# Optimization experiments

Hardware: AMD Instinct MI355X
Metric: run time of the kernel (lower is better)

## Reference

```python
import jax, jax.numpy as jnp
import numpy as np

N0, IN, HID, OUT, H = 262144, 128, 256, 256, 4
S1, S2, S3 = 32768, 4096, 512
E1, E2, E3 = 327680, 40960, 5120
NEG_SLOPE, BN_EPS = 0.2, 1e-5


def setup_inputs() -> dict:
    key = jax.random.key(0)
    ks = iter(jax.random.split(key, 64))
    def nrm(shape, fan_in):
        return jax.random.normal(next(ks), shape, jnp.float32) / np.sqrt(fan_in).astype(np.float32)
    inp = {"x": jax.random.normal(next(ks), (N0, IN), jnp.float32)}
    # (in_dim, full_out_dim, concat) per layer; per-head channels c = full/H if concat else full
    dims = [(IN, H * HID, True), (H * HID, H * HID, True), (H * HID, OUT, False)]
    for i, (din, dfull, concat) in enumerate(dims, 1):
        c = dfull // H if concat else dfull
        hc = H * c
        inp[f"w_src{i}"] = nrm((hc, din), din)
        inp[f"w_dst{i}"] = nrm((hc, din), din)
        inp[f"att_src{i}"] = nrm((H, c), c)
        inp[f"att_dst{i}"] = nrm((H, c), c)
        inp[f"b_conv{i}"] = jnp.zeros((dfull,), jnp.float32)
        inp[f"w_skip{i}"] = nrm((dfull, din), din)
        inp[f"b_skip{i}"] = jnp.zeros((dfull,), jnp.float32)
        inp[f"gamma{i}"] = jnp.ones((dfull,), jnp.float32)
        inp[f"beta{i}"] = jnp.zeros((dfull,), jnp.float32)
    for i, (E, nsrc, ndst) in enumerate([(E1, N0, S1), (E2, S1, S2), (E3, S2, S3)], 1):
        inp[f"edge_src{i}"] = jax.random.randint(next(ks), (E,), 0, nsrc, dtype=jnp.int32)
        inp[f"edge_dst{i}"] = jax.random.randint(next(ks), (E,), 0, ndst, dtype=jnp.int32)
    inp["size1"], inp["size2"], inp["size3"] = S1, S2, S3
    return inp


def gat_layer(x_all, size, src, dst, w_src, w_dst, a_src, a_dst, b, concat):
    c = w_src.shape[0] // H
    h_src = (x_all @ w_src.T).reshape(-1, H, c)        # [N_src,H,C]
    h_dst = (x_all[:size] @ w_dst.T).reshape(-1, H, c)  # [N_dst,H,C]
    al_src = jnp.einsum('nhc,hc->nh', h_src, a_src)
    al_dst = jnp.einsum('nhc,hc->nh', h_dst, a_dst)
    loop = jnp.arange(size, dtype=src.dtype)  # PyG add_self_loops on dst nodes
    s = jnp.concatenate([src, loop])
    d = jnp.concatenate([dst, loop])
    logits = jax.nn.leaky_relu(al_src[s] + al_dst[d], NEG_SLOPE)  # [E,H]
    m = jax.ops.segment_max(logits, d, num_segments=size)
    e = jnp.exp(logits - m[d])
    denom = jax.ops.segment_sum(e, d, num_segments=size)
    alpha = e / (denom[d] + 1e-16)
    out = jax.ops.segment_sum(h_src[s] * alpha[:, :, None], d, num_segments=size)
    out = out.reshape(size, H * c) if concat else out.mean(axis=1)
    return out + b


def batchnorm(x, g, b):
    mu = x.mean(0)
    var = x.var(0)
    return (x - mu) * jax.lax.rsqrt(var + BN_EPS) * g + b


def reference(x,
              w_src1, w_dst1, att_src1, att_dst1, b_conv1, w_skip1, b_skip1, gamma1, beta1,
              w_src2, w_dst2, att_src2, att_dst2, b_conv2, w_skip2, b_skip2, gamma2, beta2,
              w_src3, w_dst3, att_src3, att_dst3, b_conv3, w_skip3, b_skip3, gamma3, beta3,
              edge_src1, edge_dst1, edge_src2, edge_dst2, edge_src3, edge_dst3,
              size1, size2, size3):
    layers = [
        (size1, edge_src1, edge_dst1, w_src1, w_dst1, att_src1, att_dst1, b_conv1, w_skip1, b_skip1, gamma1, beta1, True),
        (size2, edge_src2, edge_dst2, w_src2, w_dst2, att_src2, att_dst2, b_conv2, w_skip2, b_skip2, gamma2, beta2, True),
        (size3, edge_src3, edge_dst3, w_src3, w_dst3, att_src3, att_dst3, b_conv3, w_skip3, b_skip3, gamma3, beta3, False),
    ]
    for (size, src, dst, ws, wd, a_s, a_d, bc, wsk, bsk, g, be, concat) in layers:
        x_t = x[:size]
        h = gat_layer(x, size, src, dst, ws, wd, a_s, a_d, bc, concat)
        h = h + x_t @ wsk.T + bsk
        h = batchnorm(h, g, be)
        x = jax.nn.elu(h)
    return x
```

## Files before the change

kernel.cpp:

```cpp
#include <hip/hip_runtime.h>
#include <math.h>

constexpr int N0 = 262144, S1 = 32768, S2 = 4096, S3 = 512;
constexpr int E1 = 327680, E2 = 40960, E3 = 5120;
constexpr float NEG = 0.2f, BN_EPS = 1e-5f;

typedef __attribute__((ext_vector_type(8))) short short8;
typedef __attribute__((ext_vector_type(4))) float f32x4;

__device__ __forceinline__ float lrelu(float x) { return x > 0.f ? x : NEG * x; }

__device__ __forceinline__ unsigned short f2b(float f) {
    unsigned int u = __float_as_uint(f);
    return (unsigned short)((u + 0x7FFFu + ((u >> 16) & 1u)) >> 16);
}
__device__ __forceinline__ float b2f(unsigned short u) {
    return __uint_as_float(((unsigned int)u) << 16);
}
__device__ __forceinline__ void ld4(const float* __restrict__ p, float* o) {
    float4 v = *(const float4*)p;
    o[0] = v.x; o[1] = v.y; o[2] = v.z; o[3] = v.w;
}

__device__ __forceinline__ void gload_lds16(const unsigned short* g, unsigned short* l) {
    __builtin_amdgcn_global_load_lds(
        (const __attribute__((address_space(1))) unsigned int*)g,
        (__attribute__((address_space(3))) unsigned int*)l, 16, 0, 0);
}

struct PrepArgs {
    const float* att[6]; const float* wf[6]; float* v[6];
    const float* csrc[6]; unsigned short* cdst[6];
    int* zptr; int zn4;
};

__global__ void prep_kernel(PrepArgs a)
{
    int b = blockIdx.x, t = threadIdx.x;
    if (b < 68) {
        int f, cb;
        if (b < 2)       { f = 0; cb = b; }
        else if (b < 4)  { f = 1; cb = b - 2; }
        else if (b < 20) { f = 2; cb = b - 4; }
        else if (b < 36) { f = 3; cb = b - 20; }
        else if (b < 52) { f = 4; cb = b - 36; }
        else             { f = 5; cb = b - 52; }
        int din = (f < 2) ? 128 : 1024;
        int idx = cb * 256 + t;
        int h = idx / din, k = idx - h * din;
        const float* ar = a.att[f] + h * 256;
        const float* wr = a.wf[f] + (size_t)(h * 256) * din + k;
        float acc = 0.f;
        for (int j = 0; j < 256; ++j) acc += ar[j] * wr[(size_t)j * din];
        a.v[f][idx] = acc;
    } else if (b < 124) {
        int c = b - 68, j, ob;
        if (c < 2)       { j = 0; ob = c; }
        else if (c < 4)  { j = 1; ob = c - 2; }
        else if (c < 20) { j = 2; ob = c - 4; }
        else if (c < 36) { j = 3; ob = c - 20; }
        else if (c < 40) { j = 4; ob = c - 36; }
        else             { j = 5; ob = c - 40; }
        long base = (long)ob * 65536;
        if (j < 5) {
            const float* src = a.csrc[j];
            unsigned short* dst = a.cdst[j];
            for (int it = 0; it < 64; ++it) {
                long e = base + (long)(it * 256 + t) * 4;
                float4 v = *(const float4*)(src + e);
                ushort4 u;
                u.x = f2b(v.x); u.y = f2b(v.y); u.z = f2b(v.z); u.w = f2b(v.w);
                *(ushort4*)(dst + e) = u;
            }
        } else {
            const float* src = a.csrc[5];
            unsigned short* dst = a.cdst[5];
            for (int it = 0; it < 64; ++it) {
                long e = base + (long)(it * 256 + t) * 4;
                int row = (int)(e >> 12);
                int hk = (int)(e & 4095);
                int h = hk >> 10, k = hk & 1023;
                float4 v = *(const float4*)(src + ((size_t)(h * 256 + row) << 10) + k);
                ushort4 u;
                u.x = f2b(0.25f * v.x); u.y = f2b(0.25f * v.y);
                u.z = f2b(0.25f * v.z); u.w = f2b(0.25f * v.w);
                *(ushort4*)(dst + e) = u;
            }
        }
    } else {
        int i = (b - 124) * 256 + t;
        if (i < a.zn4) ((int4*)a.zptr)[i] = make_int4(0, 0, 0, 0);
    }
}

struct CsrArgs {
    const int* edst[3];
    int* counts[3]; int* offsets[3]; int* cursor[3]; int* elist[3];
    int sizes[3];
};

__global__ void count_all(CsrArgs a)
{
    int id = blockIdx.x * 256 + threadIdx.x;
    int L, e;
    if (id < E1)           { L = 0; e = id; }
    else if (id < E1 + E2) { L = 1; e = id - E1; }
    else if (id < E1 + E2 + E3) { L = 2; e = id - E1 - E2; }
    else return;
    atomicAdd(&a.counts[L][a.edst[L][e]], 1);
}

__global__ void scan_all(CsrArgs a)
{
    __shared__ int lds[1024];
    int L = blockIdx.x;
    int size = a.sizes[L];
    const int* counts = a.counts[L];
    int* offsets = a.offsets[L];
    int* cursor = a.cursor[L];
    int t = threadIdx.x;
    int chunk = (size + 1023) >> 10;
    int begin = t * chunk;
    int end = begin + chunk; if (end > size) end = size;
    if (begin > size) begin = size;
    int s = 0;
    if ((chunk & 3) == 0) {
        for (int i = begin; i < end; i += 4) {
            int4 v = *(const int4*)(counts + i);
            s += v.x + v.y + v.z + v.w;
        }
    } else {
        for (int i = begin; i < end; ++i) s += counts[i];
    }
    lds[t] = s;
    __syncthreads();
    for (int d = 1; d < 1024; d <<= 1) {
        int v = (t >= d) ? lds[t - d] : 0;
        __syncthreads();
        lds[t] += v;
        __syncthreads();
    }
    int base = (t > 0) ? lds[t - 1] : 0;
    for (int i = begin; i < end; ++i) {
        offsets[i] = base; cursor[i] = base;
        base += counts[i];
    }
    if (t == 1023) offsets[size] = lds[1023];
}

__global__ void scatter_all(CsrArgs a)
{
    int id = blockIdx.x * 256 + threadIdx.x;
    int L, e;
    if (id < E1)           { L = 0; e = id; }
    else if (id < E1 + E2) { L = 1; e = id - E1; }
    else if (id < E1 + E2 + E3) { L = 2; e = id - E1 - E2; }
    else return;
    int p = atomicAdd(&a.cursor[L][a.edst[L][e]], 1);
    a.elist[L][p] = e;
}

__global__ void al128f_kernel(const float* __restrict__ x, const float* __restrict__ vs,
                              const float* __restrict__ vd, unsigned short* __restrict__ xb,
                              float* __restrict__ als, float* __restrict__ ald, int n, int ndst)
{
    int lane = threadIdx.x & 63;
    int wave = (blockIdx.x * 256 + threadIdx.x) >> 6;
    int nw = (gridDim.x * 256) >> 6;
    int j32 = lane & 31, half = lane >> 5;
    float vsr[4][4], vdr[4][4];
    #pragma unroll
    for (int h = 0; h < 4; ++h) {
        ld4(vs + h * 128 + j32 * 4, vsr[h]);
        ld4(vd + h * 128 + j32 * 4, vdr[h]);
    }
    for (long node = (long)wave * 2 + half; node < n; node += (long)nw * 2) {
        float4 xv = *(const float4*)(x + node * 128 + j32 * 4);
        ushort4 u;
        u.x = f2b(xv.x); u.y = f2b(xv.y); u.z = f2b(xv.z); u.w = f2b(xv.w);
        *(ushort4*)(xb + node * 128 + j32 * 4) = u;
        float xf[4] = { xv.x, xv.y, xv.z, xv.w };
        float a[4], bv[4];
        bool isd = node < ndst;
        #pragma unroll
        for (int h = 0; h < 4; ++h)
            a[h] = xf[0]*vsr[h][0] + xf[1]*vsr[h][1] + xf[2]*vsr[h][2] + xf[3]*vsr[h][3];
        if (isd) {
            #pragma unroll
            for (int h = 0; h < 4; ++h)
                bv[h] = xf[0]*vdr[h][0] + xf[1]*vdr[h][1] + xf[2]*vdr[h][2] + xf[3]*vdr[h][3];
        }
        #pragma unroll
        for (int off = 16; off > 0; off >>= 1) {
            #pragma unroll
            for (int h = 0; h < 4; ++h) a[h] += __shfl_xor(a[h], off);
            if (isd)
                #pragma unroll
                for (int h = 0; h < 4; ++h) bv[h] += __shfl_xor(bv[h], off);
        }
        if (j32 == 0) {
            *(float4*)(als + node * 4) = make_float4(a[0], a[1], a[2], a[3]);
            if (isd) *(float4*)(ald + node * 4) = make_float4(bv[0], bv[1], bv[2], bv[3]);
        }
    }
}

__global__ void al1024d_kernel(const unsigned short* __restrict__ xb,
                               const float* __restrict__ vs, const float* __restrict__ vd,
                               float* __restrict__ als, float* __restrict__ ald,
                               int nsrc, int ndst, int bsrc)
{
    bool isdst = (int)blockIdx.x >= bsrc;
    const float* v = isdst ? vd : vs;
    float* al = isdst ? ald : als;
    int n = isdst ? ndst : nsrc;
    int b0 = isdst ? blockIdx.x - bsrc : blockIdx.x;
    int nb = isdst ? gridDim.x - bsrc : bsrc;
    int lane = threadIdx.x & 63;
    int wave = (b0 * 256 + threadIdx.x) >> 6;
    int nwaves = (nb * 256) >> 6;
    float vr[4][16];
    #pragma unroll
    for (int h = 0; h < 4; ++h)
        #pragma unroll
        for (int it = 0; it < 2; ++it) {
            ld4(v + h * 1024 + it * 512 + lane * 8,     &vr[h][it * 8]);
            ld4(v + h * 1024 + it * 512 + lane * 8 + 4, &vr[h][it * 8 + 4]);
        }
    for (long node = wave; node < n; node += nwaves) {
        const unsigned short* xr = xb + node * 1024;
        float a[4] = {0.f, 0.f, 0.f, 0.f};
        #pragma unroll
        for (int it = 0; it < 2; ++it) {
            short8 u = *(const short8*)(xr + it * 512 + lane * 8);
            #pragma unroll
            for (int j = 0; j < 8; ++j) {
                float xv = b2f((unsigned short)u[j]);
                #pragma unroll
                for (int h = 0; h < 4; ++h) a[h] += xv * vr[h][it * 8 + j];
            }
        }
        #pragma unroll
        for (int off = 32; off > 0; off >>= 1)
            #pragma unroll
            for (int h = 0; h < 4; ++h) a[h] += __shfl_xor(a[h], off);
        if (lane == 0) *(float4*)(al + node * 4) = make_float4(a[0], a[1], a[2], a[3]);
    }
}

__global__ void mdnw_kernel(const float* __restrict__ als, const float* __restrict__ ald,
                            const int* __restrict__ offsets, const int* __restrict__ elist,
                            const int* __restrict__ esrc, int size,
                            float* __restrict__ aself, float* __restrict__ walpha)
{
    int d = blockIdx.x * 4 + (threadIdx.x >> 6);
    if (d >= size) return;
    int lane = threadIdx.x & 63;
    float ad[4], sl[4], q[4];
    ld4(ald + 4 * (size_t)d, ad);
    ld4(als + 4 * (size_t)d, q);
    #pragma unroll
    for (int h = 0; h < 4; ++h) sl[h] = lrelu(q[h] + ad[h]);
    int beg = offsets[d], deg = offsets[d + 1] - beg;
    float m[4] = { sl[0], sl[1], sl[2], sl[3] };
    for (int p = lane; p < deg; p += 64) {
        int s = esrc[elist[beg + p]];
        ld4(als + 4 * (size_t)s, q);
        #pragma unroll
        for (int h = 0; h < 4; ++h) m[h] = fmaxf(m[h], lrelu(q[h] + ad[h]));
    }
    #pragma unroll
    for (int off = 32; off > 0; off >>= 1)
        #pragma unroll
        for (int h = 0; h < 4; ++h) m[h] = fmaxf(m[h], __shfl_xor(m[h], off));
    float dn[4] = {0.f, 0.f, 0.f, 0.f};
    for (int p = lane; p < deg; p += 64) {
        int s = esrc[elist[beg + p]];
        ld4(als + 4 * (size_t)s, q);
        #pragma unroll
        for (int h = 0; h < 4; ++h) dn[h] += expf(lrelu(q[h] + ad[h]) - m[h]);
    }
    #pragma unroll
    for (int off = 32; off > 0; off >>= 1)
        #pragma unroll
        for (int h = 0; h < 4; ++h) dn[h] += __shfl_xor(dn[h], off);
    float r[4];
    #pragma unroll
    for (int h = 0; h < 4; ++h)
        r[h] = 1.f / (dn[h] + expf(sl[h] - m[h]) + 1e-16f);
    if (lane == 0) {
        float4 w;
        w.x = expf(sl[0] - m[0]) * r[0];
        w.y = expf(sl[1] - m[1]) * r[1];
        w.z = expf(sl[2] - m[2]) * r[2];
        w.w = expf(sl[3] - m[3]) * r[3];
        *(float4*)(aself + 4 * (size_t)d) = w;
    }
    for (int p = lane; p < deg; p += 64) {
        int e = elist[beg + p];
        int s = esrc[e];
        ld4(als + 4 * (size_t)s, q);
        float4 w;
        w.x = expf(lrelu(q[0] + ad[0]) - m[0]) * r[0];
        w.y = expf(lrelu(q[1] + ad[1]) - m[1]) * r[1];
        w.z = expf(lrelu(q[2] + ad[2]) - m[2]) * r[2];
        w.w = expf(lrelu(q[3] + ad[3]) - m[3]) * r[3];
        *(float4*)(walpha + 4 * (size_t)e) = w;
    }
}

__global__ void agg128_kernel(const unsigned short* __restrict__ xb, const float* __restrict__ walpha,
                              const float* __restrict__ aself,
                              const int* __restrict__ offsets, const int* __restrict__ elist,
                              const int* __restrict__ esrc, unsigned short* __restrict__ aggb)
{
    int d = blockIdx.x, lane = threadIdx.x;
    int beg = offsets[d], end = offsets[d + 1];
    float w[4], acc[4][2];
    ld4(aself + 4 * (size_t)d, w);
    {
        unsigned int u = *(const unsigned int*)(xb + (size_t)d * 128 + lane * 2);
        float x0 = b2f((unsigned short)(u & 0xFFFF)), x1 = b2f((unsigned short)(u >> 16));
        #pragma unroll
        for (int h = 0; h < 4; ++h) { acc[h][0] = w[h] * x0; acc[h][1] = w[h] * x1; }
    }
    for (int p = beg; p < end; ++p) {
        int e = elist[p];
        int s = esrc[e];
        ld4(walpha + 4 * (size_t)e, w);
        unsigned int u = *(const unsigned int*)(xb + (size_t)s * 128 + lane * 2);
        float x0 = b2f((unsigned short)(u & 0xFFFF)), x1 = b2f((unsigned short)(u >> 16));
        #pragma unroll
        for (int h = 0; h < 4; ++h) { acc[h][0] += w[h] * x0; acc[h][1] += w[h] * x1; }
    }
    unsigned int* og = (unsigned int*)(aggb + (size_t)d * 512);
    #pragma unroll
    for (int h = 0; h < 4; ++h)
        og[h * 64 + lane] = (unsigned int)f2b(acc[h][0]) | ((unsigned int)f2b(acc[h][1]) << 16);
}

__global__ void agg1024_kernel(const unsigned short* __restrict__ xb, const float* __restrict__ walpha,
                               const float* __restrict__ aself,
                               const int* __restrict__ offsets, const int* __restrict__ elist,
                               const int* __restrict__ esrc, unsigned short* __restrict__ aggb)
{
    int d = blockIdx.x, t = threadIdx.x;
    int beg = offsets[d], end = offsets[d + 1];
    float w[4], acc[4][4];
    ld4(aself + 4 * (size_t)d, w);
    {
        ushort4 u = *(const ushort4*)(xb + (size_t)d * 1024 + t * 4);
        float xv[4] = { b2f(u.x), b2f(u.y), b2f(u.z), b2f(u.w) };
        #pragma unroll
        for (int h = 0; h < 4; ++h)
            #pragma unroll
            for (int j = 0; j < 4; ++j) acc[h][j] = w[h] * xv[j];
    }
    for (int p = beg; p < end; ++p) {
        int e = elist[p];
        int s = esrc[e];
        ld4(walpha + 4 * (size_t)e, w);
        ushort4 u = *(const ushort4*)(xb + (size_t)s * 1024 + t * 4);
        float xv[4] = { b2f(u.x), b2f(u.y), b2f(u.z), b2f(u.w) };
        #pragma unroll
        for (int h = 0; h < 4; ++h)
            #pragma unroll
            for (int j = 0; j < 4; ++j) acc[h][j] += w[h] * xv[j];
    }
    unsigned short* og = aggb + (size_t)d * 4096;
    #pragma unroll
    for (int h = 0; h < 4; ++h) {
        ushort4 u;
        u.x = f2b(acc[h][0]); u.y = f2b(acc[h][1]);
        u.z = f2b(acc[h][2]); u.w = f2b(acc[h][3]);
        *(ushort4*)(og + h * 1024 + t * 4) = u;
    }
}

#define SWZ(r, c) ((((c) ^ (((r) >> 1) & 3)) << 3))

template<int BM, int BN>
__global__ __launch_bounds__(256) void gemm2_kernel(
    const unsigned short* __restrict__ A1, int lda1, const unsigned short* __restrict__ W1, int K1,
    const unsigned short* __restrict__ A2, int lda2, const unsigned short* __restrict__ W2, int K2,
    int hs2, int cph2,
    unsigned short* __restrict__ C, int N,
    float* __restrict__ bnsum, float* __restrict__ bnsq)
{
    constexpr int WM = BM / 2, WN = BN / 2;
    constexpr int TM = WM / 16, TN = WN / 16;
    constexpr int APASS = (BM * 4) / 256, BPASS = (BN * 4) / 256;
    __shared__ __align__(16) unsigned short As[BM * 32];
    __shared__ __align__(16) unsigned short Bs[BN * 32];
    __shared__ float sbn[2 * BN];
    int tid = threadIdx.x;
    int n0 = blockIdx.x * BN, m0 = blockIdx.y * BM;
    int l = tid & 63, l16 = l & 15, kq = l >> 4;
    int wid = tid >> 6, wr = wid >> 1, wc = wid & 1;

    f32x4 acc[TM][TN];
    #pragma unroll
    for (int mi = 0; mi < TM; ++mi)
        #pragma unroll
        for (int ni = 0; ni < TN; ++ni) acc[mi][ni] = (f32x4){0.f, 0.f, 0.f, 0.f};

    #pragma unroll
    for (int ph = 0; ph < 2; ++ph) {
        const unsigned short* Ap = ph ? A2 + (size_t)m0 * lda2 + (cph2 ? (size_t)(n0 / cph2) * hs2 : 0)
                                      : A1 + (size_t)m0 * lda1;
        int lda = ph ? lda2 : lda1;
        const unsigned short* Wp = ph ? W2 + (size_t)n0 * K2 : W1 + (size_t)n0 * K1;
        int ldw = ph ? K2 : K1;
        int K = ph ? K2 : K1;
        for (int k0 = 0; k0 < K; k0 += 32) {
            #pragma unroll
            for (int ps = 0; ps < APASS; ++ps) {
                int sbase = ps * 256 + wid * 64;
                int s = sbase + l;
                int r = s >> 2, cc = s & 3;
                gload_lds16(Ap + (size_t)r * lda + k0 + ((cc ^ ((r >> 1) & 3)) << 3),
                            &As[(size_t)sbase * 8]);
            }
            #pragma unroll
            for (int ps = 0; ps < BPASS; ++ps) {
                int sbase = ps * 256 + wid * 64;
                int s = sbase + l;
                int r = s >> 2, cc = s & 3;
                gload_lds16(Wp + (size_t)r * ldw + k0 + ((cc ^ ((r >> 1) & 3)) << 3),
                            &Bs[(size_t)sbase * 8]);
            }
            __syncthreads();
            short8 af[TM], bfr[TN];
            #pragma unroll
            for (int mi = 0; mi < TM; ++mi) {
                int r = wr * WM + mi * 16 + l16;
                af[mi] = *(const short8*)&As[r * 32 + SWZ(r, kq)];
            }
            #pragma unroll
            for (int ni = 0; ni < TN; ++ni) {
                int r = wc * WN + ni * 16 + l16;
                bfr[ni] = *(const short8*)&Bs[r * 32 + SWZ(r, kq)];
            }
            #pragma unroll
            for (int mi = 0; mi < TM; ++mi)
                #pragma unroll
                for (int ni = 0; ni < TN; ++ni)
                    acc[mi][ni] = __builtin_amdgcn_mfma_f32_16x16x32_bf16(
                        af[mi], bfr[ni], acc[mi][ni], 0, 0, 0);
            __syncthreads();
        }
    }

    if (tid < 2 * BN) sbn[tid] = 0.f;
    __syncthreads();

    #pragma unroll
    for (int ni = 0; ni < TN; ++ni) {
        int col = wc * WN + ni * 16 + l16;
        float s = 0.f, q = 0.f;
        #pragma unroll
        for (int mi = 0; mi < TM; ++mi) {
            int rowb = wr * WM + mi * 16 + (kq << 2);
            #pragma unroll
            for (int r = 0; r < 4; ++r) {
                float v = acc[mi][ni][r];
                C[(size_t)(m0 + rowb + r) * N + n0 + col] = f2b(v);
                s += v; q += v * v;
            }
        }
        atomicAdd(&sbn[col * 2 + 0], s);
        atomicAdd(&sbn[col * 2 + 1], q);
    }
    __syncthreads();
    if (tid < BN) {
        atomicAdd(&bnsum[n0 + tid], sbn[tid * 2 + 0]);
        atomicAdd(&bnsq[n0 + tid], sbn[tid * 2 + 1]);
    }
}

__global__ __launch_bounds__(256) void gemm3_splitk(
    const unsigned short* __restrict__ A1, const unsigned short* __restrict__ W1,
    const unsigned short* __restrict__ A2, const unsigned short* __restrict__ W2,
    float* __restrict__ Cpart)
{
    constexpr int BM = 64, BN = 64, WM = 32, WN = 32, TM = 2, TN = 2;
    __shared__ __align__(16) unsigned short As[BM * 32];
    __shared__ __align__(16) unsigned short Bs[BN * 32];
    int tid = threadIdx.x;
    int n0 = blockIdx.x * BN, m0 = blockIdx.y * BM;
    int z = blockIdx.z;
    int ph = (z >= 2);
    int ks = ph ? (z - 2) * 512 : z * 512;
    const unsigned short* Ap = ph ? A2 + (size_t)m0 * 4096 : A1 + (size_t)m0 * 1024;
    const unsigned short* Wp = ph ? W2 + (size_t)n0 * 4096 : W1 + (size_t)n0 * 1024;
    int lda = ph ? 4096 : 1024;
    int l = tid & 63, l16 = l & 15, kq = l >> 4;
    int wid = tid >> 6, wr = wid >> 1, wc = wid & 1;

    f32x4 acc[TM][TN];
    #pragma unroll
    for (int mi = 0; mi < TM; ++mi)
        #pragma unroll
        for (int ni = 0; ni < TN; ++ni) acc[mi][ni] = (f32x4){0.f, 0.f, 0.f, 0.f};

    for (int k0 = ks; k0 < ks + 512; k0 += 32) {
        {
            int sbase = wid * 64;
            int s = sbase + l;
            int r = s >> 2, cc = s & 3;
            gload_lds16(Ap + (size_t)r * lda + k0 + ((cc ^ ((r >> 1) & 3)) << 3),
                        &As[(size_t)sbase * 8]);
            gload_lds16(Wp + (size_t)r * lda + k0 + ((cc ^ ((r >> 1) & 3)) << 3),
                        &Bs[(size_t)sbase * 8]);
        }
        __syncthreads();
        short8 af[TM], bfr[TN];
        #pragma unroll
        for (int mi = 0; mi < TM; ++mi) {
            int r = wr * WM + mi * 16 + l16;
            af[mi] = *(const short8*)&As[r * 32 + SWZ(r, kq)];
        }
        #pragma unroll
        for (int ni = 0; ni < TN; ++ni) {
            int r = wc * WN + ni * 16 + l16;
            bfr[ni] = *(const short8*)&Bs[r * 32 + SWZ(r, kq)];
        }
        #pragma unroll
        for (int mi = 0; mi < TM; ++mi)
            #pragma unroll
            for (int ni = 0; ni < TN; ++ni)
                acc[mi][ni] = __builtin_amdgcn_mfma_f32_16x16x32_bf16(
                    af[mi], bfr[ni], acc[mi][ni], 0, 0, 0);
        __syncthreads();
    }

    float* Cz = Cpart + (size_t)z * S3 * 256;
    #pragma unroll
    for (int ni = 0; ni < TN; ++ni) {
        int col = wc * WN + ni * 16 + l16;
        #pragma unroll
        for (int mi = 0; mi < TM; ++mi) {
            int rowb = wr * WM + mi * 16 + (kq << 2);
            #pragma unroll
            for (int r = 0; r < 4; ++r)
                Cz[(size_t)(m0 + rowb + r) * 256 + n0 + col] = acc[mi][ni][r];
        }
    }
}

__global__ void bnstat3_kernel(const float* __restrict__ Cpart, float* __restrict__ hb32,
                               float* __restrict__ bnsum, float* __restrict__ bnsq)
{
    int c = threadIdx.x;
    int r0 = blockIdx.x * 64;
    float s = 0.f, q = 0.f;
    for (int r = r0; r < r0 + 64; ++r) {
        float v = 0.f;
        #pragma unroll
        for (int z = 0; z < 10; ++z)
            v += Cpart[((size_t)z * S3 + r) * 256 + c];
        hb32[(size_t)r * 256 + c] = v;
        s += v; q += v * v;
    }
    atomicAdd(&bnsum[c], s);
    atomicAdd(&bnsq[c], q);
}

__global__ void norm_elu_bb(const unsigned short* __restrict__ h,
                            const float* __restrict__ sum, const float* __restrict__ sq,
                            const float* __restrict__ gamma, const float* __restrict__ beta,
                            unsigned short* __restrict__ out, int N, float invM, long total)
{
    long i = ((long)blockIdx.x * 256 + threadIdx.x) * 4;
    if (i >= total) return;
    int c = (int)(i % N);
    float4 sm = *(const float4*)(sum + c);
    float4 qq = *(const float4*)(sq + c);
    float4 gm = *(const float4*)(gamma + c);
    float4 bt = *(const float4*)(beta + c);
    float mu0 = sm.x * invM, mu1 = sm.y * invM, mu2 = sm.z * invM, mu3 = sm.w * invM;
    float sc0 = gm.x * rsqrtf(qq.x * invM - mu0 * mu0 + BN_EPS);
    float sc1 = gm.y * rsqrtf(qq.y * invM - mu1 * mu1 + BN_EPS);
    float sc2 = gm.z * rsqrtf(qq.z * invM - mu2 * mu2 + BN_EPS);
    float sc3 = gm.w * rsqrtf(qq.w * invM - mu3 * mu3 + BN_EPS);
    float sh0 = bt.x - mu0 * sc0, sh1 = bt.y - mu1 * sc1;
    float sh2 = bt.z - mu2 * sc2, sh3 = bt.w - mu3 * sc3;
    ushort4 u = *(const ushort4*)(h + i);
    float v0 = b2f(u.x) * sc0 + sh0;
    float v1 = b2f(u.y) * sc1 + sh1;
    float v2 = b2f(u.z) * sc2 + sh2;
    float v3 = b2f(u.w) * sc3 + sh3;
    v0 = v0 > 0.f ? v0 : expm1f(v0);
    v1 = v1 > 0.f ? v1 : expm1f(v1);
    v2 = v2 > 0.f ? v2 : expm1f(v2);
    v3 = v3 > 0.f ? v3 : expm1f(v3);
    ushort4 o;
    o.x = f2b(v0); o.y = f2b(v1); o.z = f2b(v2); o.w = f2b(v3);
    *(ushort4*)(out + i) = o;
}

__global__ void norm_elu_ff(const float* __restrict__ h,
                            const float* __restrict__ sum, const float* __restrict__ sq,
                            const float* __restrict__ gamma, const float* __restrict__ beta,
                            float* __restrict__ out, int N, float invM, long total)
{
    long i = ((long)blockIdx.x * 256 + threadIdx.x) * 4;
    if (i >= total) return;
    int c = (int)(i % N);
    float4 sm = *(const float4*)(sum + c);
    float4 qq = *(const float4*)(sq + c);
    float4 gm = *(const float4*)(gamma + c);
    float4 bt = *(const float4*)(beta + c);
    float mu0 = sm.x * invM, mu1 = sm.y * invM, mu2 = sm.z * invM, mu3 = sm.w * invM;
    float sc0 = gm.x * rsqrtf(qq.x * invM - mu0 * mu0 + BN_EPS);
    float sc1 = gm.y * rsqrtf(qq.y * invM - mu1 * mu1 + BN_EPS);
    float sc2 = gm.z * rsqrtf(qq.z * invM - mu2 * mu2 + BN_EPS);
    float sc3 = gm.w * rsqrtf(qq.w * invM - mu3 * mu3 + BN_EPS);
    float4 hv = *(const float4*)(h + i);
    float4 o;
    o.x = hv.x * sc0 + (bt.x - mu0 * sc0);
    o.y = hv.y * sc1 + (bt.y - mu1 * sc1);
    o.z = hv.z * sc2 + (bt.z - mu2 * sc2);
    o.w = hv.w * sc3 + (bt.w - mu3 * sc3);
    o.x = o.x > 0.f ? o.x : expm1f(o.x);
    o.y = o.y > 0.f ? o.y : expm1f(o.y);
    o.z = o.z > 0.f ? o.z : expm1f(o.z);
    o.w = o.w > 0.f ? o.w : expm1f(o.w);
    *(float4*)(out + i) = o;
}

extern "C" void kernel_launch(void* const* d_in, const int* in_sizes, int n_in,
                              void* d_out, int out_size, void* d_ws, size_t ws_size,
                              hipStream_t stream)
{
    const float* x = (const float*)d_in[0];
    auto P = [&](int layer, int slot) -> const float* {
        return (const float*)d_in[1 + (layer - 1) * 9 + slot];
    };
    const int* edge_src[3] = { (const int*)d_in[28], (const int*)d_in[30], (const int*)d_in[32] };
    const int* edge_dst[3] = { (const int*)d_in[29], (const int*)d_in[31], (const int*)d_in[33] };

    char* wsb = (char*)d_ws;
    size_t off = 0;
    auto alloc = [&](size_t bytes) -> void* {
        void* p = wsb + off;
        off = (off + bytes + 255) & ~(size_t)255;
        return p;
    };
    unsigned short* xb0   = (unsigned short*)alloc((size_t)N0 * 128 * 2);
    unsigned short* x1b   = (unsigned short*)alloc((size_t)S1 * 1024 * 2);
    unsigned short* x2b   = (unsigned short*)alloc((size_t)S2 * 1024 * 2);
    unsigned short* hb    = (unsigned short*)alloc((size_t)S1 * 1024 * 2);
    unsigned short* aggb  = (unsigned short*)alloc((size_t)S2 * 4096 * 2);
    unsigned short* wskipb[3] = {
        (unsigned short*)alloc(131072 * 2),
        (unsigned short*)alloc(1048576 * 2),
        (unsigned short*)alloc(262144 * 2) };
    unsigned short* wsrcb[3] = {
        (unsigned short*)alloc(131072 * 2),
        (unsigned short*)alloc(1048576 * 2),
        (unsigned short*)alloc(1048576 * 2) };
    float* vbuf[6];
    vbuf[0] = (float*)alloc(512 * 4);
    vbuf[1] = (float*)alloc(512 * 4);
    vbuf[2] = (float*)alloc(4096 * 4);
    vbuf[3] = (float*)alloc(4096 * 4);
    vbuf[4] = (float*)alloc(4096 * 4);
    vbuf[5] = (float*)alloc(4096 * 4);
    float* als     = (float*)alloc((size_t)N0 * 4 * 4);
    float* ald     = (float*)alloc((size_t)S1 * 4 * 4);
    float* aself   = (float*)alloc((size_t)S1 * 4 * 4);
    float* walpha  = (float*)alloc((size_t)E1 * 4 * 4);
    float* Cpart   = (float*)alloc((size_t)10 * S3 * 256 * 4);
    float* hb32    = (float*)alloc((size_t)S3 * 256 * 4);
    int* offsets3[3] = { (int*)alloc((S1 + 1) * 4), (int*)alloc((S2 + 1) * 4), (int*)alloc((S3 + 1) * 4) };
    int* cursor3 [3] = { (int*)alloc(S1 * 4), (int*)alloc(S2 * 4), (int*)alloc(S3 * 4) };
    int* elist3  [3] = { (int*)alloc(E1 * 4), (int*)alloc(E2 * 4), (int*)alloc(E3 * 4) };
    int zn = S1 + S2 + S3 + 6 * 1024;
    int* zreg = (int*)alloc((size_t)zn * 4);
    int* counts[3] = { zreg, zreg + S1, zreg + S1 + S2 };
    float* bnsum[3] = { (float*)(zreg + S1 + S2 + S3),
                        (float*)(zreg + S1 + S2 + S3 + 2048),
                        (float*)(zreg + S1 + S2 + S3 + 4096) };
    float* bnsq[3]  = { bnsum[0] + 1024, bnsum[1] + 1024, bnsum[2] + 1024 };

    PrepArgs pa;
    for (int L = 0; L < 3; ++L) {
        pa.att[2 * L]     = P(L + 1, 2); pa.wf[2 * L]     = P(L + 1, 0); pa.v[2 * L]     = vbuf[2 * L];
        pa.att[2 * L + 1] = P(L + 1, 3); pa.wf[2 * L + 1] = P(L + 1, 1); pa.v[2 * L + 1] = vbuf[2 * L + 1];
    }
    pa.csrc[0] = P(1, 5); pa.cdst[0] = wskipb[0];
    pa.csrc[1] = P(1, 0); pa.cdst[1] = wsrcb[0];
    pa.csrc[2] = P(2, 5); pa.cdst[2] = wskipb[1];
    pa.csrc[3] = P(2, 0); pa.cdst[3] = wsrcb[1];
    pa.csrc[4] = P(3, 5); pa.cdst[4] = wskipb[2];
    pa.csrc[5] = P(3, 0); pa.cdst[5] = wsrcb[2];
    pa.zptr = zreg; pa.zn4 = zn / 4;
    prep_kernel<<<167, 256, 0, stream>>>(pa);

    CsrArgs ca;
    for (int L = 0; L < 3; ++L) {
        ca.edst[L] = edge_dst[L];
        ca.counts[L] = counts[L]; ca.offsets[L] = offsets3[L];
        ca.cursor[L] = cursor3[L]; ca.elist[L] = elist3[L];
    }
    ca.sizes[0] = S1; ca.sizes[1] = S2; ca.sizes[2] = S3;
    count_all<<<(E1 + E2 + E3) / 256, 256, 0, stream>>>(ca);
    scan_all<<<3, 1024, 0, stream>>>(ca);
    scatter_all<<<(E1 + E2 + E3) / 256, 256, 0, stream>>>(ca);

    al128f_kernel<<<2048, 256, 0, stream>>>(x, vbuf[0], vbuf[1], xb0, als, ald, N0, S1);
    mdnw_kernel<<<(S1 + 3) / 4, 256, 0, stream>>>(als, ald, offsets3[0], elist3[0], edge_src[0],
                                                  S1, aself, walpha);
    agg128_kernel<<<S1, 64, 0, stream>>>(xb0, walpha, aself, offsets3[0], elist3[0], edge_src[0], aggb);
    gemm2_kernel<128, 128><<<dim3(1024 / 128, S1 / 128), 256, 0, stream>>>(
        xb0, 128, wskipb[0], 128,
        aggb, 512, wsrcb[0], 128, 128, 256,
        hb, 1024, bnsum[0], bnsq[0]);
    norm_elu_bb<<<(int)(((long)S1 * 1024 / 4 + 255) / 256), 256, 0, stream>>>(
        hb, bnsum[0], bnsq[0], P(1, 7), P(1, 8), x1b, 1024, 1.f / S1, (long)S1 * 1024);

    al1024d_kernel<<<576, 256, 0, stream>>>(x1b, vbuf[2], vbuf[3], als, ald, S1, S2, 512);
    mdnw_kernel<<<(S2 + 3) / 4, 256, 0, stream>>>(als, ald, offsets3[1], elist3[1], edge_src[1],
                                                  S2, aself, walpha);
    agg1024_kernel<<<S2, 256, 0, stream>>>(x1b, walpha, aself, offsets3[1], elist3[1], edge_src[1], aggb);
    gemm2_kernel<64, 64><<<dim3(1024 / 64, S2 / 64), 256, 0, stream>>>(
        x1b, 1024, wskipb[1], 1024,
        aggb, 4096, wsrcb[1], 1024, 1024, 256,
        hb, 1024, bnsum[1], bnsq[1]);
    norm_elu_bb<<<(int)(((long)S2 * 1024 / 4 + 255) / 256), 256, 0, stream>>>(
        hb, bnsum[1], bnsq[1], P(2, 7), P(2, 8), x2b, 1024, 1.f / S2, (long)S2 * 1024);

    al1024d_kernel<<<72, 256, 0, stream>>>(x2b, vbuf[4], vbuf[5], als, ald, S2, S3, 64);
    mdnw_kernel<<<(S3 + 3) / 4, 256, 0, stream>>>(als, ald, offsets3[2], elist3[2], edge_src[2],
                                                  S3, aself, walpha);
    agg1024_kernel<<<S3, 256, 0, stream>>>(x2b, walpha, aself, offsets3[2], elist3[2], edge_src[2], aggb);
    gemm3_splitk<<<dim3(256 / 64, S3 / 64, 10), 256, 0, stream>>>(
        x2b, wskipb[2], aggb, wsrcb[2], Cpart);
    bnstat3_kernel<<<8, 256, 0, stream>>>(Cpart, hb32, bnsum[2], bnsq[2]);
    norm_elu_ff<<<(int)(((long)S3 * 256 / 4 + 255) / 256), 256, 0, stream>>>(
        hb32, bnsum[2], bnsq[2], P(3, 7), P(3, 8), (float*)d_out, 256, 1.f / S3, (long)S3 * 256);
}
```

Baseline: 539.6 us.

## Store source ids in CSR, swizzle GEMM tile order, widen norm-ELU per thread

The CSR scatter now writes each edge's source node id directly in place of the edge id. This removes the double indirection esrc[elist[p]] in the softmax and aggregation kernels. Attention weights are stored in CSR order, so aggregation reads them contiguously instead of by scattered edge index. Separately, the GEMM block index is swizzled in groups of 8, likely to spread neighbouring tiles across XCDs for cache locality, and norm_elu_bb handles 8 elements per thread with half the grid.

```diff
diff --git a/kernel.cpp b/kernel.cpp
--- a/kernel.cpp
+++ b/kernel.cpp
@@ -94,8 +94,8 @@
 }
 
 struct CsrArgs {
-    const int* edst[3];
-    int* counts[3]; int* offsets[3]; int* cursor[3]; int* elist[3];
+    const int* edst[3]; const int* esrc[3];
+    int* counts[3]; int* offsets[3]; int* cursor[3]; int* slist[3];
     int sizes[3];
 };
 
@@ -157,7 +157,7 @@
     else if (id < E1 + E2 + E3) { L = 2; e = id - E1 - E2; }
     else return;
     int p = atomicAdd(&a.cursor[L][a.edst[L][e]], 1);
-    a.elist[L][p] = e;
+    a.slist[L][p] = a.esrc[L][e];
 }
 
 __global__ void al128f_kernel(const float* __restrict__ x, const float* __restrict__ vs,
@@ -249,9 +249,8 @@
 }
 
 __global__ void mdnw_kernel(const float* __restrict__ als, const float* __restrict__ ald,
-                            const int* __restrict__ offsets, const int* __restrict__ elist,
-                            const int* __restrict__ esrc, int size,
-                            float* __restrict__ aself, float* __restrict__ walpha)
+                            const int* __restrict__ offsets, const int* __restrict__ slist,
+                            int size, float* __restrict__ aself, float* __restrict__ walpha)
 {
     int d = blockIdx.x * 4 + (threadIdx.x >> 6);
     if (d >= size) return;
@@ -264,7 +263,7 @@
     int beg = offsets[d], deg = offsets[d + 1] - beg;
     float m[4] = { sl[0], sl[1], sl[2], sl[3] };
     for (int p = lane; p < deg; p += 64) {
-        int s = esrc[elist[beg + p]];
+        int s = slist[beg + p];
         ld4(als + 4 * (size_t)s, q);
         #pragma unroll
         for (int h = 0; h < 4; ++h) m[h] = fmaxf(m[h], lrelu(q[h] + ad[h]));
@@ -275,7 +274,7 @@
         for (int h = 0; h < 4; ++h) m[h] = fmaxf(m[h], __shfl_xor(m[h], off));
     float dn[4] = {0.f, 0.f, 0.f, 0.f};
     for (int p = lane; p < deg; p += 64) {
-        int s = esrc[elist[beg + p]];
+        int s = slist[beg + p];
         ld4(als + 4 * (size_t)s, q);
         #pragma unroll
         for (int h = 0; h < 4; ++h) dn[h] += expf(lrelu(q[h] + ad[h]) - m[h]);
@@ -297,22 +296,21 @@
         *(float4*)(aself + 4 * (size_t)d) = w;
     }
     for (int p = lane; p < deg; p += 64) {
-        int e = elist[beg + p];
-        int s = esrc[e];
+        int s = slist[beg + p];
         ld4(als + 4 * (size_t)s, q);
         float4 w;
         w.x = expf(lrelu(q[0] + ad[0]) - m[0]) * r[0];
         w.y = expf(lrelu(q[1] + ad[1]) - m[1]) * r[1];
         w.z = expf(lrelu(q[2] + ad[2]) - m[2]) * r[2];
         w.w = expf(lrelu(q[3] + ad[3]) - m[3]) * r[3];
-        *(float4*)(walpha + 4 * (size_t)e) = w;
+        *(float4*)(walpha + 4 * (size_t)(beg + p)) = w;
     }
 }
 
 __global__ void agg128_kernel(const unsigned short* __restrict__ xb, const float* __restrict__ walpha,
                               const float* __restrict__ aself,
-                              const int* __restrict__ offsets, const int* __restrict__ elist,
-                              const int* __restrict__ esrc, unsigned short* __restrict__ aggb)
+                              const int* __restrict__ offsets, const int* __restrict__ slist,
+                              unsigned short* __restrict__ aggb)
 {
     int d = blockIdx.x, lane = threadIdx.x;
     int beg = offsets[d], end = offsets[d + 1];
@@ -325,9 +323,8 @@
         for (int h = 0; h < 4; ++h) { acc[h][0] = w[h] * x0; acc[h][1] = w[h] * x1; }
     }
     for (int p = beg; p < end; ++p) {
-        int e = elist[p];
-        int s = esrc[e];
-        ld4(walpha + 4 * (size_t)e, w);
+        int s = slist[p];
+        ld4(walpha + 4 * (size_t)p, w);
         unsigned int u = *(const unsigned int*)(xb + (size_t)s * 128 + lane * 2);
         float x0 = b2f((unsigned short)(u & 0xFFFF)), x1 = b2f((unsigned short)(u >> 16));
         #pragma unroll
@@ -341,8 +338,8 @@
 
 __global__ void agg1024_kernel(const unsigned short* __restrict__ xb, const float* __restrict__ walpha,
                                const float* __restrict__ aself,
-                               const int* __restrict__ offsets, const int* __restrict__ elist,
-                               const int* __restrict__ esrc, unsigned short* __restrict__ aggb)
+                               const int* __restrict__ offsets, const int* __restrict__ slist,
+                               unsigned short* __restrict__ aggb)
 {
     int d = blockIdx.x, t = threadIdx.x;
     int beg = offsets[d], end = offsets[d + 1];
@@ -357,9 +354,8 @@
             for (int j = 0; j < 4; ++j) acc[h][j] = w[h] * xv[j];
     }
     for (int p = beg; p < end; ++p) {
-        int e = elist[p];
-        int s = esrc[e];
-        ld4(walpha + 4 * (size_t)e, w);
+        int s = slist[p];
+        ld4(walpha + 4 * (size_t)p, w);
         ushort4 u = *(const ushort4*)(xb + (size_t)s * 1024 + t * 4);
         float xv[4] = { b2f(u.x), b2f(u.y), b2f(u.z), b2f(u.w) };
         #pragma unroll
@@ -394,7 +390,12 @@
     __shared__ __align__(16) unsigned short Bs[BN * 32];
     __shared__ float sbn[2 * BN];
     int tid = threadIdx.x;
-    int n0 = blockIdx.x * BN, m0 = blockIdx.y * BM;
+    int gx = gridDim.x;
+    int nwg = gx * gridDim.y;
+    int bid = blockIdx.y * gx + blockIdx.x;
+    int cpx = nwg >> 3;
+    int swz = (bid & 7) * cpx + (bid >> 3);
+    int n0 = (swz % gx) * BN, m0 = (swz / gx) * BM;
     int l = tid & 63, l16 = l & 15, kq = l >> 4;
     int wid = tid >> 6, wr = wid >> 1, wc = wid & 1;
 
@@ -571,32 +572,36 @@
                             const float* __restrict__ gamma, const float* __restrict__ beta,
                             unsigned short* __restrict__ out, int N, float invM, long total)
 {
-    long i = ((long)blockIdx.x * 256 + threadIdx.x) * 4;
-    if (i >= total) return;
-    int c = (int)(i % N);
-    float4 sm = *(const float4*)(sum + c);
-    float4 qq = *(const float4*)(sq + c);
-    float4 gm = *(const float4*)(gamma + c);
-    float4 bt = *(const float4*)(beta + c);
-    float mu0 = sm.x * invM, mu1 = sm.y * invM, mu2 = sm.z * invM, mu3 = sm.w * invM;
-    float sc0 = gm.x * rsqrtf(qq.x * invM - mu0 * mu0 + BN_EPS);
-    float sc1 = gm.y * rsqrtf(qq.y * invM - mu1 * mu1 + BN_EPS);
-    float sc2 = gm.z * rsqrtf(qq.z * invM - mu2 * mu2 + BN_EPS);
-    float sc3 = gm.w * rsqrtf(qq.w * invM - mu3 * mu3 + BN_EPS);
-    float sh0 = bt.x - mu0 * sc0, sh1 = bt.y - mu1 * sc1;
-    float sh2 = bt.z - mu2 * sc2, sh3 = bt.w - mu3 * sc3;
-    ushort4 u = *(const ushort4*)(h + i);
-    float v0 = b2f(u.x) * sc0 + sh0;
-    float v1 = b2f(u.y) * sc1 + sh1;
-    float v2 = b2f(u.z) * sc2 + sh2;
-    float v3 = b2f(u.w) * sc3 + sh3;
-    v0 = v0 > 0.f ? v0 : expm1f(v0);
-    v1 = v1 > 0.f ? v1 : expm1f(v1);
-    v2 = v2 > 0.f ? v2 : expm1f(v2);
-    v3 = v3 > 0.f ? v3 : expm1f(v3);
-    ushort4 o;
-    o.x = f2b(v0); o.y = f2b(v1); o.z = f2b(v2); o.w = f2b(v3);
-    *(ushort4*)(out + i) = o;
+    long i0 = ((long)blockIdx.x * 256 + threadIdx.x) * 8;
+    if (i0 >= total) return;
+    #pragma unroll
+    for (int g = 0; g < 2; ++g) {
+        long i = i0 + g * 4;
+        int c = (int)(i % N);
+        float4 sm = *(const float4*)(sum + c);
+        float4 qq = *(const float4*)(sq + c);
+        float4 gm = *(const float4*)(gamma + c);
+        float4 bt = *(const float4*)(beta + c);
+        float mu0 = sm.x * invM, mu1 = sm.y * invM, mu2 = sm.z * invM, mu3 = sm.w * invM;
+        float sc0 = gm.x * rsqrtf(qq.x * invM - mu0 * mu0 + BN_EPS);
+        float sc1 = gm.y * rsqrtf(qq.y * invM - mu1 * mu1 + BN_EPS);
+        float sc2 = gm.z * rsqrtf(qq.z * invM - mu2 * mu2 + BN_EPS);
+        float sc3 = gm.w * rsqrtf(qq.w * invM - mu3 * mu3 + BN_EPS);
+        float sh0 = bt.x - mu0 * sc0, sh1 = bt.y - mu1 * sc1;
+        float sh2 = bt.z - mu2 * sc2, sh3 = bt.w - mu3 * sc3;
+        ushort4 u = *(const ushort4*)(h + i);
+        float v0 = b2f(u.x) * sc0 + sh0;
+        float v1 = b2f(u.y) * sc1 + sh1;
+        float v2 = b2f(u.z) * sc2 + sh2;
+        float v3 = b2f(u.w) * sc3 + sh3;
+        v0 = v0 > 0.f ? v0 : expm1f(v0);
+        v1 = v1 > 0.f ? v1 : expm1f(v1);
+        v2 = v2 > 0.f ? v2 : expm1f(v2);
+        v3 = v3 > 0.f ? v3 : expm1f(v3);
+        ushort4 o;
+        o.x = f2b(v0); o.y = f2b(v1); o.z = f2b(v2); o.w = f2b(v3);
+        *(ushort4*)(out + i) = o;
+    }
 }
 
 __global__ void norm_elu_ff(const float* __restrict__ h,
@@ -675,7 +680,7 @@
     float* hb32    = (float*)alloc((size_t)S3 * 256 * 4);
     int* offsets3[3] = { (int*)alloc((S1 + 1) * 4), (int*)alloc((S2 + 1) * 4), (int*)alloc((S3 + 1) * 4) };
     int* cursor3 [3] = { (int*)alloc(S1 * 4), (int*)alloc(S2 * 4), (int*)alloc(S3 * 4) };
-    int* elist3  [3] = { (int*)alloc(E1 * 4), (int*)alloc(E2 * 4), (int*)alloc(E3 * 4) };
+    int* slist3  [3] = { (int*)alloc(E1 * 4), (int*)alloc(E2 * 4), (int*)alloc(E3 * 4) };
     int zn = S1 + S2 + S3 + 6 * 1024;
     int* zreg = (int*)alloc((size_t)zn * 4);
     int* counts[3] = { zreg, zreg + S1, zreg + S1 + S2 };
@@ -700,9 +705,9 @@
 
     CsrArgs ca;
     for (int L = 0; L < 3; ++L) {
-        ca.edst[L] = edge_dst[L];
+        ca.edst[L] = edge_dst[L]; ca.esrc[L] = edge_src[L];
         ca.counts[L] = counts[L]; ca.offsets[L] = offsets3[L];
-        ca.cursor[L] = cursor3[L]; ca.elist[L] = elist3[L];
+        ca.cursor[L] = cursor3[L]; ca.slist[L] = slist3[L];
     }
     ca.sizes[0] = S1; ca.sizes[1] = S2; ca.sizes[2] = S3;
     count_all<<<(E1 + E2 + E3) / 256, 256, 0, stream>>>(ca);
@@ -710,31 +715,28 @@
     scatter_all<<<(E1 + E2 + E3) / 256, 256, 0, stream>>>(ca);
 
     al128f_kernel<<<2048, 256, 0, stream>>>(x, vbuf[0], vbuf[1], xb0, als, ald, N0, S1);
-    mdnw_kernel<<<(S1 + 3) / 4, 256, 0, stream>>>(als, ald, offsets3[0], elist3[0], edge_src[0],
-                                                  S1, aself, walpha);
-    agg128_kernel<<<S1, 64, 0, stream>>>(xb0, walpha, aself, offsets3[0], elist3[0], edge_src[0], aggb);
+    mdnw_kernel<<<(S1 + 3) / 4, 256, 0, stream>>>(als, ald, offsets3[0], slist3[0], S1, aself, walpha);
+    agg128_kernel<<<S1, 64, 0, stream>>>(xb0, walpha, aself, offsets3[0], slist3[0], aggb);
     gemm2_kernel<128, 128><<<dim3(1024 / 128, S1 / 128), 256, 0, stream>>>(
         xb0, 128, wskipb[0], 128,
         aggb, 512, wsrcb[0], 128, 128, 256,
         hb, 1024, bnsum[0], bnsq[0]);
-    norm_elu_bb<<<(int)(((long)S1 * 1024 / 4 + 255) / 256), 256, 0, stream>>>(
+    norm_elu_bb<<<(int)(((long)S1 * 1024 / 8 + 255) / 256), 256, 0, stream>>>(
         hb, bnsum[0], bnsq[0], P(1, 7), P(1, 8), x1b, 1024, 1.f / S1, (long)S1 * 1024);
 
     al1024d_kernel<<<576, 256, 0, stream>>>(x1b, vbuf[2], vbuf[3], als, ald, S1, S2, 512);
-    mdnw_kernel<<<(S2 + 3) / 4, 256, 0, stream>>>(als, ald, offsets3[1], elist3[1], edge_src[1],
-                                                  S2, aself, walpha);
-    agg1024_kernel<<<S2, 256, 0, stream>>>(x1b, walpha, aself, offsets3[1], elist3[1], edge_src[1], aggb);
+    mdnw_kernel<<<(S2 + 3) / 4, 256, 0, stream>>>(als, ald, offsets3[1], slist3[1], S2, aself, walpha);
+    agg1024_kernel<<<S2, 256, 0, stream>>>(x1b, walpha, aself, offsets3[1], slist3[1], aggb);
     gemm2_kernel<64, 64><<<dim3(1024 / 64, S2 / 64), 256, 0, stream>>>(
         x1b, 1024, wskipb[1], 1024,
         aggb, 4096, wsrcb[1], 1024, 1024, 256,
         hb, 1024, bnsum[1], bnsq[1]);
-    norm_elu_bb<<<(int)(((long)S2 * 1024 / 4 + 255) / 256), 256, 0, stream>>>(
+    norm_elu_bb<<<(int)(((long)S2 * 1024 / 8 + 255) / 256), 256, 0, stream>>>(
         hb, bnsum[1], bnsq[1], P(2, 7), P(2, 8), x2b, 1024, 1.f / S2, (long)S2 * 1024);
 
     al1024d_kernel<<<72, 256, 0, stream>>>(x2b, vbuf[4], vbuf[5], als, ald, S2, S3, 64);
-    mdnw_kernel<<<(S3 + 3) / 4, 256, 0, stream>>>(als, ald, offsets3[2], elist3[2], edge_src[2],
-                                                  S3, aself, walpha);
-    agg1024_kernel<<<S3, 256, 0, stream>>>(x2b, walpha, aself, offsets3[2], elist3[2], edge_src[2], aggb);
+    mdnw_kernel<<<(S3 + 3) / 4, 256, 0, stream>>>(als, ald, offsets3[2], slist3[2], S3, aself, walpha);
+    agg1024_kernel<<<S3, 256, 0, stream>>>(x2b, walpha, aself, offsets3[2], slist3[2], aggb);
     gemm3_splitk<<<dim3(256 / 64, S3 / 64, 10), 256, 0, stream>>>(
         x2b, wskipb[2], aggb, wsrcb[2], Cpart);
     bnstat3_kernel<<<8, 256, 0, stream>>>(Cpart, hb32, bnsum[2], bnsq[2]);
```

Result: faster. 508.2 us (-5.8%).
